# Optimization experiments

Measured on AMD Instinct MI355X. Metric: run time of the kernel, lower is better.

## Reference

```python
import jax, jax.numpy as jnp
import numpy as np
from jax import lax

KERNEL = 3
CIN = 512
FMAPS = 512
LATENT = 512
GAIN = 1.0
LRMUL = 1.0
# StyleGAN2 wscale: runtime_coef = gain / sqrt(fan_in) * lrmul
RC_W = GAIN / np.sqrt(KERNEL * KERNEL * CIN) * LRMUL
RC_S = GAIN / np.sqrt(LATENT) * LRMUL


def setup_inputs() -> dict:
    key = jax.random.key(0)
    k1, k2, k3, k4, k5 = jax.random.split(key, 5)
    N, H, W = 8, 64, 64
    x = jax.random.normal(k1, (N, CIN, H, W), dtype=jnp.float32)
    dlatent_vect = jax.random.normal(k2, (N, LATENT), dtype=jnp.float32)
    weight = jax.random.normal(k3, (KERNEL, KERNEL, CIN, FMAPS), dtype=jnp.float32)
    mod_weight = jax.random.normal(k4, (LATENT, CIN), dtype=jnp.float32)
    mod_bias = jax.random.normal(k5, (CIN,), dtype=jnp.float32)
    return {"x": x, "dlatent_vect": dlatent_vect, "weight": weight,
            "mod_weight": mod_weight, "mod_bias": mod_bias}


def reference(x, dlatent_vect, weight, mod_weight, mod_bias):
    N, _, H, W = x.shape
    w = weight * RC_W                                       # [kh,kw,Cin,Cout]
    # style: s = A(dlatent) + 1
    s = dlatent_vect @ (mod_weight * RC_S) + mod_bias * LRMUL + 1.0  # [N,Cin]
    # per-sample modulated weights
    ww = w[None] * s[:, None, None, :, None]                # [N,kh,kw,Cin,Cout]
    # demodulate
    d = lax.rsqrt(jnp.sum(jnp.square(ww), axis=(1, 2, 3)) + 1e-8)  # [N,Cout]
    ww = ww * d[:, None, None, None, :]
    # fused modconv: one grouped conv with N groups
    xr = x.reshape(1, N * CIN, H, W)
    wr = jnp.transpose(ww, (1, 2, 3, 0, 4)).reshape(KERNEL, KERNEL, CIN, N * FMAPS)
    out = lax.conv_general_dilated(
        xr, wr, window_strides=(1, 1), padding="SAME",
        dimension_numbers=("NCHW", "HWIO", "NCHW"),
        feature_group_count=N)
    return out.reshape(N, FMAPS, H, W)
```

## Files before the change

kernel.cpp:

```cpp
#include <hip/hip_runtime.h>
#include <math.h>

#define CIN_    512
#define COUT_   512
#define LATENT_ 512
#define NB_     8
#define HH_     64
#define WW_     64

typedef float f32x16 __attribute__((ext_vector_type(16)));
typedef short bf16x8v __attribute__((ext_vector_type(8)));

__device__ inline unsigned short f2bf(float f) {
    union { float f; unsigned u; } v; v.f = f;
    unsigned r = v.u + 0x7fffu + ((v.u >> 16) & 1u);
    return (unsigned short)(r >> 16);
}

__device__ __forceinline__ void gl_lds16(const void* g, void* l) {
    __builtin_amdgcn_global_load_lds(
        (const __attribute__((address_space(1))) unsigned int*)g,
        (__attribute__((address_space(3))) unsigned int*)l,
        16, 0, 0);
}

__global__ __launch_bounds__(256) void prep1(
    const float* __restrict__ w, const float* __restrict__ dlat,
    const float* __restrict__ mw, const float* __restrict__ mb,
    float* __restrict__ wsq, unsigned short* __restrict__ wb,
    float* __restrict__ s)
{
    __shared__ float smem[16 * 521];
    const float RC_W = 0.0147313912747197f;
    const float RC_S = 0.0441941738241592f;
    int b = blockIdx.x;
    int t = threadIdx.x;

    if (b < 1024) {
        int idx = b * 256 + t;
        float acc = 0.f;
#pragma unroll
        for (int tap = 0; tap < 9; ++tap) {
            float v = w[tap * (CIN_ * COUT_) + idx];
            acc += v * v;
        }
        wsq[idx] = acc;
    } else if (b < 1312) {
        int bb  = b - 1024;
        int tap = bb / 32;
        int cb  = bb % 32;
        for (int idx = t; idx < 16 * 512; idx += 256) {
            int ci = idx >> 9;
            int co = idx & 511;
            smem[ci * 521 + co] = w[((size_t)tap * 512 + cb * 16 + ci) * 512 + co];
        }
        __syncthreads();
        unsigned short* dst = wb + (size_t)(tap * 32 + cb) * 1024 * 8;
        for (int p = t; p < 2048; p += 256) {
            int l  = (p >> 1) & 63;
            int g  = p >> 7;
            int co = g * 32 + (l & 31);
            int ci = (l >> 5) * 8 + (p & 1) * 4;
            ushort4 o4;
            o4.x = f2bf(smem[(ci + 0) * 521 + co] * RC_W);
            o4.y = f2bf(smem[(ci + 1) * 521 + co] * RC_W);
            o4.z = f2bf(smem[(ci + 2) * 521 + co] * RC_W);
            o4.w = f2bf(smem[(ci + 3) * 521 + co] * RC_W);
            *(ushort4*)&dst[p * 4] = o4;
        }
    } else {
        int bb  = b - 1312;
        int n   = bb >> 3;
        int ci0 = (bb & 7) * 64;
        for (int i = t; i < LATENT_; i += 256) smem[i] = dlat[n * LATENT_ + i];
        __syncthreads();
        int cil  = t & 63;
        int part = t >> 6;
        const float* mwp = mw + ci0 + cil;
        float a0 = 0.f, a1 = 0.f;
        int l0 = part * 128;
#pragma unroll 4
        for (int l = l0; l < l0 + 128; l += 2) {
            a0 += smem[l]     * mwp[(size_t)l * CIN_];
            a1 += smem[l + 1] * mwp[(size_t)(l + 1) * CIN_];
        }
        smem[512 + part * 64 + cil] = a0 + a1;
        __syncthreads();
        if (t < 64) {
            float r = smem[512 + t] + smem[576 + t] + smem[640 + t] + smem[704 + t];
            s[n * CIN_ + ci0 + t] = r * RC_S + mb[ci0 + t] + 1.0f;
        }
    }
}

__global__ __launch_bounds__(256) void prep2(
    const float* __restrict__ x, const float* __restrict__ s,
    const float* __restrict__ wsq, float* __restrict__ dmod,
    unsigned short* __restrict__ xt)
{
    __shared__ float smem[16 * 67 + 16];
    int b = blockIdx.x;
    int t = threadIdx.x;

    if (b < 64) {
        const float RCW2 = 1.0f / 4608.0f;
        int n   = b >> 3;
        int co0 = (b & 7) * 64;
        for (int i = t; i < CIN_; i += 256) { float v = s[n * CIN_ + i]; smem[i] = v * v; }
        __syncthreads();
        int col  = t & 63;
        int part = t >> 6;
        const float* wp = wsq + co0 + col;
        float a0 = 0.f, a1 = 0.f;
        int c0 = part * 128;
#pragma unroll 4
        for (int ci = c0; ci < c0 + 128; ci += 2) {
            a0 += smem[ci]     * wp[(size_t)ci * COUT_];
            a1 += smem[ci + 1] * wp[(size_t)(ci + 1) * COUT_];
        }
        smem[512 + part * 64 + col] = a0 + a1;
        __syncthreads();
        if (t < 64) {
            float r = smem[512 + t] + smem[576 + t] + smem[640 + t] + smem[704 + t];
            dmod[n * COUT_ + co0 + t] = rsqrtf(RCW2 * r + 1e-8f);
        }
    } else {
        int bb = b - 64;
        int rg = bb % 6;
        int cb = (bb / 6) % 32;
        int n  = bb / (6 * 32);

        if (t < 16) smem[16 * 67 + t] = s[n * CIN_ + cb * 16 + t];

        for (int hp = rg * 11; hp < rg * 11 + 11; ++hp) {
            int gh = hp - 1;
            bool rowok = (gh >= 0) && (gh < HH_);
            if (rowok) {
                const float* src = &x[(((size_t)n * CIN_ + cb * 16) * HH_ + gh) * WW_];
                int ci = t >> 4;
                int g0 = (t & 15) * 4;
                float4 v = *(const float4*)&src[(size_t)ci * (HH_ * WW_) + g0];
                float* dstl = &smem[ci * 67 + g0];
                dstl[0] = v.x; dstl[1] = v.y; dstl[2] = v.z; dstl[3] = v.w;
            }
            __syncthreads();

            unsigned short* dst = xt + (((size_t)(n * 32 + cb) * 66 + hp) * 66) * 16;
            for (int p = t; p < 264; p += 256) {
                int e   = p * 4;
                int wp_ = e >> 4;
                int cie = e & 15;
                int gw  = wp_ - 1;
                float vv0 = 0.f, vv1 = 0.f, vv2 = 0.f, vv3 = 0.f;
                if (rowok && gw >= 0 && gw < WW_) {
                    vv0 = smem[(cie + 0) * 67 + gw] * smem[16 * 67 + cie + 0];
                    vv1 = smem[(cie + 1) * 67 + gw] * smem[16 * 67 + cie + 1];
                    vv2 = smem[(cie + 2) * 67 + gw] * smem[16 * 67 + cie + 2];
                    vv3 = smem[(cie + 3) * 67 + gw] * smem[16 * 67 + cie + 3];
                }
                ushort4 o4;
                o4.x = f2bf(vv0); o4.y = f2bf(vv1); o4.z = f2bf(vv2); o4.w = f2bf(vv3);
                *(ushort4*)&dst[e] = o4;
            }
            __syncthreads();
        }
    }
}

__global__ __launch_bounds__(256, 2) void conv_mfma(
    const unsigned short* __restrict__ xt,
    const unsigned short* __restrict__ wb,
    const float* __restrict__ dmod,
    float* __restrict__ out)
{
    __shared__ __align__(16) union {
        struct { unsigned short xs[2880]; unsigned short ws[36864]; } s;
        float o[64 * 129];
    } sm;

    int b   = blockIdx.x;
    int cot = b & 1;
    int wt_ = (b >> 1) & 3;
    int ht  = (b >> 3) & 7;
    int n   = b >> 6;
    int h0 = ht * 8, w0 = wt_ * 16, co0 = cot * 256;

    int t    = threadIdx.x;
    int wv   = t >> 6, lane = t & 63;
    int mh   = wv >> 1, nh = wv & 1;
    int l5   = lane & 31, half = lane >> 5;

    f32x16 acc[2][4];
#pragma unroll
    for (int ms = 0; ms < 2; ++ms)
#pragma unroll
        for (int ns = 0; ns < 4; ++ns)
#pragma unroll
            for (int i = 0; i < 16; ++i) acc[ms][ns][i] = 0.f;

    for (int cb = 0; cb < 32; ++cb) {
        const unsigned short* xb = xt + (((size_t)(n * 32 + cb) * 66 + h0) * 66 + w0) * 16;
        {
            int li = t;
            int m  = li ^ ((li >> 3) & 7);
            gl_lds16(&xb[(m / 36) * 1056 + (m % 36) * 8], &sm.s.xs[(li & ~63) * 8]);
            li = t + 256;
            if (li < 360) {
                m = li ^ ((li >> 3) & 7);
                gl_lds16(&xb[(m / 36) * 1056 + (m % 36) * 8], &sm.s.xs[(li & ~63) * 8]);
            }
        }
        const unsigned short* wbb = wb + ((size_t)cb * 1024 + cot * 512) * 8;
#pragma unroll
        for (int tap = 0; tap < 9; ++tap) {
            const unsigned short* tsrc = wbb + (size_t)tap * 32 * 1024 * 8;
            gl_lds16(&tsrc[t * 8],         &sm.s.ws[tap * 4096 + (t & ~63) * 8]);
            gl_lds16(&tsrc[(t + 256) * 8], &sm.s.ws[tap * 4096 + ((t + 256) & ~63) * 8]);
        }
        __syncthreads();

#pragma unroll
        for (int tap = 0; tap < 9; ++tap) {
            int kh = tap / 3, kw = tap - 3 * (tap / 3);
            bf16x8v bfr[4], afr[2];
#pragma unroll
            for (int ns = 0; ns < 4; ++ns) {
                bfr[ns] = *(const bf16x8v*)&sm.s.ws[tap * 4096 + ((nh * 4 + ns) * 64 + lane) * 8];
            }
#pragma unroll
            for (int ms = 0; ms < 2; ++ms) {
                int pr = mh * 4 + ms * 2 + (l5 >> 4);
                int pc = l5 & 15;
                int pos = (pr + kh) * 18 + (pc + kw);
                int ch  = pos * 2 + half;
                ch ^= (ch >> 3) & 7;
                afr[ms] = *(const bf16x8v*)&sm.s.xs[ch * 8];
            }
#pragma unroll
            for (int ms = 0; ms < 2; ++ms)
#pragma unroll
                for (int ns = 0; ns < 4; ++ns)
                    acc[ms][ns] = __builtin_amdgcn_mfma_f32_32x32x16_bf16(
                        afr[ms], bfr[ns], acc[ms][ns], 0, 0, 0);
        }
        __syncthreads();
    }

    for (int p = 0; p < 4; ++p) {
        __syncthreads();
        if (nh == (p >> 1)) {
#pragma unroll
            for (int q = 0; q < 2; ++q) {
                int bco = q * 32 + l5;
                float dv = dmod[n * COUT_ + co0 + p * 64 + bco];
#pragma unroll
                for (int ms = 0; ms < 2; ++ms) {
#pragma unroll
                    for (int reg = 0; reg < 16; ++reg) {
                        int ml = (reg & 3) + 8 * (reg >> 2) + 4 * half;
                        int m  = mh * 64 + ms * 32 + ml;
                        sm.o[bco * 129 + m] = acc[ms][(p & 1) * 2 + q][reg] * dv;
                    }
                }
            }
        }
        __syncthreads();
        for (int j = t; j < 2048; j += 256) {
            int wq = j & 3;
            int pairidx = j >> 2;
            int row  = pairidx & 7;
            int bco2 = pairidx >> 3;
            int co = co0 + p * 64 + bco2;
            const float* src = &sm.o[bco2 * 129 + row * 16 + wq * 4];
            float4 v = make_float4(src[0], src[1], src[2], src[3]);
            *(float4*)&out[(((size_t)n * COUT_ + co) * HH_ + h0 + row) * WW_ + w0 + wq * 4] = v;
        }
    }
}

extern "C" void kernel_launch(void* const* d_in, const int* in_sizes, int n_in,
                              void* d_out, int out_size, void* d_ws, size_t ws_size,
                              hipStream_t stream) {
    const float* x    = (const float*)d_in[0];
    const float* dlat = (const float*)d_in[1];
    const float* w    = (const float*)d_in[2];
    const float* mw   = (const float*)d_in[3];
    const float* mb   = (const float*)d_in[4];
    float* out = (float*)d_out;

    char* ws = (char*)d_ws;
    float* s    = (float*)(ws);
    float* dmod = (float*)(ws + 16384);
    float* wsq  = (float*)(ws + 32768);
    unsigned short* xt = (unsigned short*)(ws + 1081344);
    unsigned short* wb = (unsigned short*)(ws + 36765696);

    prep1<<<1376, 256, 0, stream>>>(w, dlat, mw, mb, wsq, wb, s);
    prep2<<<64 + NB_ * 32 * 6, 256, 0, stream>>>(x, s, wsq, dmod, xt);
    conv_mfma<<<512, 256, 0, stream>>>(xt, wb, dmod, out);
}
```

Baseline: 264.6 us.

## Software-pipeline weight taps and input tiles with triple/double-buffered LDS

Replaces the load-all-then-compute-per-channel-block loop with a per-tap pipeline. Weight taps are prefetched two ahead into a 3-slot LDS ring, and the input tile is double-buffered and prefetched mid-block. Explicit vmcnt waits and barriers replace the full syncthreads. MFMA sections run at raised priority. The goal is to hide global-to-LDS load latency behind MFMA work and to shrink LDS use, which may allow more occupancy. The cost is a barrier after every tap and fragile hand-counted waitcnt values.

```diff
diff --git a/kernel.cpp b/kernel.cpp
--- a/kernel.cpp
+++ b/kernel.cpp
@@ -174,7 +174,10 @@
     float* __restrict__ out)
 {
     __shared__ __align__(16) union {
-        struct { unsigned short xs[2880]; unsigned short ws[36864]; } s;
+        struct {
+            unsigned short xs[2][512 * 8];
+            unsigned short ws[3][4096];
+        } s;
         float o[64 * 129];
     } sm;
 
@@ -190,6 +193,15 @@
     int mh   = wv >> 1, nh = wv & 1;
     int l5   = lane & 31, half = lane >> 5;
 
+    const int wsrc0 = t * 8, wsrc1 = (t + 256) * 8;
+    const int wdst0 = (t & ~63) * 8, wdst1 = ((t + 256) & ~63) * 8;
+    int m0 = t ^ ((t >> 3) & 7);
+    int li1 = t + 256;
+    int m1 = li1 ^ ((li1 >> 3) & 7); if (m1 > 359) m1 = 359;
+    const int xsrc0 = (m0 / 36) * 1056 + (m0 % 36) * 8;
+    const int xsrc1 = (m1 / 36) * 1056 + (m1 % 36) * 8;
+    const int xdst0 = (t & ~63) * 8, xdst1 = ((t + 256) & ~63) * 8;
+
     f32x16 acc[2][4];
 #pragma unroll
     for (int ms = 0; ms < 2; ++ms)
@@ -198,35 +210,38 @@
 #pragma unroll
             for (int i = 0; i < 16; ++i) acc[ms][ns][i] = 0.f;
 
+    auto stage_ws = [&](int cb2, int tap2, int q) {
+        const unsigned short* tsrc = wb + ((size_t)(tap2 * 32 + cb2) * 1024 + cot * 512) * 8;
+        unsigned short* d = (unsigned short*)sm.s.ws[q];
+        gl_lds16(&tsrc[wsrc0], &d[wdst0]);
+        gl_lds16(&tsrc[wsrc1], &d[wdst1]);
+    };
+    auto stage_xs = [&](int cb2, int bq) {
+        const unsigned short* xb2 = xt + (((size_t)(n * 32 + cb2) * 66 + h0) * 66 + w0) * 16;
+        unsigned short* d = (unsigned short*)sm.s.xs[bq];
+        gl_lds16(&xb2[xsrc0], &d[xdst0]);
+        gl_lds16(&xb2[xsrc1], &d[xdst1]);
+    };
+
+    stage_ws(0, 0, 0);
+    stage_ws(0, 1, 1);
+    stage_xs(0, 0);
+    asm volatile("s_waitcnt vmcnt(0)" ::: "memory");
+    __builtin_amdgcn_s_barrier();
+
     for (int cb = 0; cb < 32; ++cb) {
-        const unsigned short* xb = xt + (((size_t)(n * 32 + cb) * 66 + h0) * 66 + w0) * 16;
-        {
-            int li = t;
-            int m  = li ^ ((li >> 3) & 7);
-            gl_lds16(&xb[(m / 36) * 1056 + (m % 36) * 8], &sm.s.xs[(li & ~63) * 8]);
-            li = t + 256;
-            if (li < 360) {
-                m = li ^ ((li >> 3) & 7);
-                gl_lds16(&xb[(m / 36) * 1056 + (m % 36) * 8], &sm.s.xs[(li & ~63) * 8]);
-            }
-        }
-        const unsigned short* wbb = wb + ((size_t)cb * 1024 + cot * 512) * 8;
+        const unsigned short* xsb = (const unsigned short*)sm.s.xs[cb & 1];
 #pragma unroll
         for (int tap = 0; tap < 9; ++tap) {
-            const unsigned short* tsrc = wbb + (size_t)tap * 32 * 1024 * 8;
-            gl_lds16(&tsrc[t * 8],         &sm.s.ws[tap * 4096 + (t & ~63) * 8]);
-            gl_lds16(&tsrc[(t + 256) * 8], &sm.s.ws[tap * 4096 + ((t + 256) & ~63) * 8]);
-        }
-        __syncthreads();
-
-#pragma unroll
-        for (int tap = 0; tap < 9; ++tap) {
-            int kh = tap / 3, kw = tap - 3 * (tap / 3);
+            const int p  = tap % 3;
+            const int q2 = (tap + 2) % 3;
+            const int kh = tap / 3, kw = tap % 3;
+
             bf16x8v bfr[4], afr[2];
-#pragma unroll
-            for (int ns = 0; ns < 4; ++ns) {
-                bfr[ns] = *(const bf16x8v*)&sm.s.ws[tap * 4096 + ((nh * 4 + ns) * 64 + lane) * 8];
-            }
+            const unsigned short* wsb = (const unsigned short*)sm.s.ws[p];
+#pragma unroll
+            for (int ns = 0; ns < 4; ++ns)
+                bfr[ns] = *(const bf16x8v*)&wsb[((nh * 4 + ns) * 64 + lane) * 8];
 #pragma unroll
             for (int ms = 0; ms < 2; ++ms) {
                 int pr = mh * 4 + ms * 2 + (l5 >> 4);
@@ -234,32 +249,51 @@
                 int pos = (pr + kh) * 18 + (pc + kw);
                 int ch  = pos * 2 + half;
                 ch ^= (ch >> 3) & 7;
-                afr[ms] = *(const bf16x8v*)&sm.s.xs[ch * 8];
-            }
+                afr[ms] = *(const bf16x8v*)&xsb[ch * 8];
+            }
+
+            {
+                int tap2 = tap + 2, cb2 = cb;
+                if (tap2 >= 9) { tap2 -= 9; cb2 = cb + 1; }
+                if (cb2 > 31) cb2 = 31;
+                stage_ws(cb2, tap2, q2);
+            }
+            if (tap == 4) {
+                int cb2 = (cb + 1 > 31) ? 31 : cb + 1;
+                stage_xs(cb2, (cb + 1) & 1);
+            }
+
+            __builtin_amdgcn_s_setprio(1);
 #pragma unroll
             for (int ms = 0; ms < 2; ++ms)
 #pragma unroll
                 for (int ns = 0; ns < 4; ++ns)
                     acc[ms][ns] = __builtin_amdgcn_mfma_f32_32x32x16_bf16(
                         afr[ms], bfr[ns], acc[ms][ns], 0, 0, 0);
-        }
-        __syncthreads();
+            __builtin_amdgcn_s_setprio(0);
+
+            if (tap == 4) asm volatile("s_waitcnt vmcnt(4)" ::: "memory");
+            else          asm volatile("s_waitcnt vmcnt(2)" ::: "memory");
+            __builtin_amdgcn_s_barrier();
+        }
     }
 
-    for (int p = 0; p < 4; ++p) {
-        __syncthreads();
-        if (nh == (p >> 1)) {
+    asm volatile("s_waitcnt vmcnt(0)" ::: "memory");
+
+    for (int pss = 0; pss < 4; ++pss) {
+        __syncthreads();
+        if (nh == (pss >> 1)) {
 #pragma unroll
             for (int q = 0; q < 2; ++q) {
                 int bco = q * 32 + l5;
-                float dv = dmod[n * COUT_ + co0 + p * 64 + bco];
+                float dv = dmod[n * COUT_ + co0 + pss * 64 + bco];
 #pragma unroll
                 for (int ms = 0; ms < 2; ++ms) {
 #pragma unroll
                     for (int reg = 0; reg < 16; ++reg) {
                         int ml = (reg & 3) + 8 * (reg >> 2) + 4 * half;
                         int m  = mh * 64 + ms * 32 + ml;
-                        sm.o[bco * 129 + m] = acc[ms][(p & 1) * 2 + q][reg] * dv;
+                        sm.o[bco * 129 + m] = acc[ms][(pss & 1) * 2 + q][reg] * dv;
                     }
                 }
             }
@@ -270,7 +304,7 @@
             int pairidx = j >> 2;
             int row  = pairidx & 7;
             int bco2 = pairidx >> 3;
-            int co = co0 + p * 64 + bco2;
+            int co = co0 + pss * 64 + bco2;
             const float* src = &sm.o[bco2 * 129 + row * 16 + wq * 4];
             float4 v = make_float4(src[0], src[1], src[2], src[3]);
             *(float4*)&out[(((size_t)n * COUT_ + co) * HH_ + h0 + row) * WW_ + w0 + wq * 4] = v;
```

New measurement: 257.4 us. -2.7%, faster.
